# Optimization experiments

Hardware: AMD Instinct MI355X
Metric: run time of the kernel (lower is better)

Reference implementation:

```python
import jax, jax.numpy as jnp
import numpy as np

K = 16  # number of nearest neighbors


def setup_inputs() -> dict:
    key = jax.random.key(0)
    k1, k2, k3 = jax.random.split(key, 3)
    B, N, C, C_OUT = 2, 8192, 64, 64
    coords_knn = jax.random.normal(k1, (B, N, 3), dtype=jnp.float32)
    feat = jax.random.normal(k2, (B, N, C), dtype=jnp.float32)
    # MLP params: Linear(2*C + 3 -> C_OUT)
    W = jax.random.normal(k3, (2 * C + 3, C_OUT), dtype=jnp.float32) * 0.05
    b = jnp.zeros((C_OUT,), dtype=jnp.float32)
    return {"coords_knn": coords_knn, "feat": feat, "W": W, "b": b}


def _knn_idx(coords, k):
    # pairwise squared distances: ||xi||^2 + ||xj||^2 - 2 xi.xj   -> [B, N, N]
    xx = jnp.sum(coords ** 2, axis=-1, keepdims=True)
    dist = xx + jnp.swapaxes(xx, 1, 2) - 2.0 * jnp.einsum('bnc,bmc->bnm', coords, coords)
    dist = jnp.maximum(dist, 0.0)
    _, idx = jax.lax.top_k(-dist, k)  # k smallest distances (order irrelevant: max-pool)
    return idx  # [B, N, k] int32


def reference(coords_knn, feat, W, b):
    idx = _knn_idx(coords_knn, K)
    gather = jax.vmap(lambda a, i: a[i])          # per-batch gather: [N,C],[N,k] -> [N,k,C]
    nb_f = gather(feat, idx)                      # [B, N, k, C]
    nb_p = gather(coords_knn, idx)                # [B, N, k, 3]
    fi = feat[:, :, None, :]                      # [B, N, 1, C]
    pi = coords_knn[:, :, None, :]                # [B, N, 1, 3]
    x = jnp.concatenate(
        [jnp.broadcast_to(fi, nb_f.shape), nb_f - fi, nb_p - pi], axis=-1
    )                                             # [B, N, k, 2C+3]
    x = jax.nn.relu(jnp.einsum('bnkd,do->bnko', x, W) + b)
    return jnp.max(x, axis=2)                     # [B, N, C_OUT]
```

## Files before the change

### kernel.cpp

```cpp
#include <hip/hip_runtime.h>
#include <hip/hip_bf16.h>
#include <stdint.h>
#include <float.h>

#define B_ 2
#define N_ 8192
#define C_ 64
#define K_ 16
#define D_IN 131
#define XS_STRIDE 168
#define TS 1024
#define QPB 16
#define QPW 4
#define CAP 128

typedef __attribute__((ext_vector_type(8))) short short8v;
typedef __attribute__((ext_vector_type(4))) float f32x4;

#define SENT_U64 0x7F7FFFFFFFFFFFFFull

__device__ __forceinline__ float sq3(float x, float y, float z) {
#pragma clang fp contract(off)
  return (x * x + y * y) + z * z;
}

__device__ __forceinline__ uint64_t shfl_xor_u64(uint64_t x, int mask) {
  int lo = __shfl_xor((int)(uint32_t)(x & 0xffffffffull), mask, 64);
  int hi = __shfl_xor((int)(uint32_t)(x >> 32), mask, 64);
  return ((uint64_t)(uint32_t)hi << 32) | (uint32_t)lo;
}

__device__ __forceinline__ double shfl_xor_f64(double x, int mask) {
  return __builtin_bit_cast(double, shfl_xor_u64(__builtin_bit_cast(uint64_t, x), mask));
}

__device__ __forceinline__ uint64_t pack_key_u64(float d, int idx) {
  return ((uint64_t)__float_as_uint(d) << 32) | (uint32_t)idx;
}

__device__ __forceinline__ void insert16(double* hd, double key) {
  hd[15] = key;
#pragma unroll
  for (int z = 15; z >= 1; --z) {
    double a = hd[z - 1], b = hd[z];
    hd[z - 1] = fmin(a, b);
    hd[z] = fmax(a, b);
  }
}

__device__ __forceinline__ float exact_d(float qx, float qy, float qz, float xxq,
                                         float4 cd) {
  float dot2 = fmaf(qz, cd.z, fmaf(qy, cd.y, qx * cd.x));
  float dtmp;
  {
#pragma clang fp contract(off)
    dtmp = (xxq + cd.w) - dot2;
  }
  return fmaxf(dtmp, 0.0f);
}

__global__ __launch_bounds__(256) void prep_c(const float* __restrict__ coords,
                                              float4* __restrict__ c4) {
  int i = blockIdx.x * 256 + threadIdx.x;
  if (i >= B_ * N_) return;
  float cx = coords[i * 3 + 0], cy = coords[i * 3 + 1], cz = coords[i * 3 + 2];
  c4[i] = make_float4(2.0f * cx, 2.0f * cy, 2.0f * cz, sq3(cx, cy, cz));
}

__global__ __launch_bounds__(256) void knn_kernel(const float* __restrict__ coords,
                                                  const float4* __restrict__ c4,
                                                  int* __restrict__ idxout) {
  __shared__ float4 cl[TS];
  __shared__ unsigned long long sbuf[QPB][CAP];
  __shared__ int scnt[QPB];
  const int t = threadIdx.x;
  const int w = t >> 6;
  const int lane = t & 63;
  const int blk = blockIdx.x;
  const int bb = blk >> 9;
  const int qbase = (blk & 511) * QPB;
  const float* cb = coords + (size_t)bb * N_ * 3;
  const float4* cg = c4 + (size_t)bb * N_;

  float qx[QPW], qy[QPW], qz[QPW], xxq[QPW];
#pragma unroll
  for (int r = 0; r < QPW; ++r) {
    int n = qbase + w * QPW + r;
    qx[r] = cb[n * 3 + 0]; qy[r] = cb[n * 3 + 1]; qz[r] = cb[n * 3 + 2];
    xxq[r] = sq3(qx[r], qy[r], qz[r]);
  }
  if (t < QPB) scnt[t] = 0;

#define PROXY(r, cd) fmaf(qz[r], (cd).z, fmaf(qy[r], (cd).y, fmaf(qx[r], (cd).x, -(cd).w)))

  float M[QPW];
#pragma unroll
  for (int r = 0; r < QPW; ++r) M[r] = -FLT_MAX;

  for (int j0 = 0; j0 < N_; j0 += TS) {
    __syncthreads();
#pragma unroll
    for (int i = 0; i < TS / 256; ++i) cl[t + 256 * i] = cg[j0 + t + 256 * i];
    __syncthreads();
#pragma unroll
    for (int i = 0; i < TS / 64; i += 2) {
      float4 ca = cl[i * 64 + lane];
      float4 cb2 = cl[(i + 1) * 64 + lane];
#pragma unroll
      for (int r = 0; r < QPW; ++r) {
        float pa = PROXY(r, ca);
        float pb = PROXY(r, cb2);
        M[r] = fmaxf(M[r], fmaxf(pa, pb));
      }
    }
  }

  float A[QPW], pT[QPW];
#pragma unroll
  for (int r = 0; r < QPW; ++r) { A[r] = M[r]; pT[r] = -FLT_MAX; }
#pragma unroll
  for (int rd = 0; rd < 16; ++rd) {
#pragma unroll
    for (int r = 0; r < QPW; ++r) {
      float g = A[r];
      g = fmaxf(g, __shfl_xor(g, 1, 64));
      g = fmaxf(g, __shfl_xor(g, 2, 64));
      g = fmaxf(g, __shfl_xor(g, 4, 64));
      g = fmaxf(g, __shfl_xor(g, 8, 64));
      g = fmaxf(g, __shfl_xor(g, 16, 64));
      g = fmaxf(g, __shfl_xor(g, 32, 64));
      pT[r] = g;
      A[r] = (A[r] == g) ? -FLT_MAX : A[r];
    }
  }
  float X[QPW];
#pragma unroll
  for (int r = 0; r < QPW; ++r) {
    float slop = 6e-6f * (fabsf(xxq[r]) + fabsf(pT[r])) + 1e-5f;
    X[r] = fminf(pT[r], xxq[r]) - 2.0f * slop;
  }

  for (int j0 = 0; j0 < N_; j0 += TS) {
    __syncthreads();
#pragma unroll
    for (int i = 0; i < TS / 256; ++i) cl[t + 256 * i] = cg[j0 + t + 256 * i];
    __syncthreads();
#pragma unroll
    for (int i = 0; i < TS / 64; i += 2) {
      const int ia = j0 + i * 64 + lane;
      const int ib = ia + 64;
      float4 ca = cl[i * 64 + lane];
      float4 cb2 = cl[(i + 1) * 64 + lane];
#pragma unroll
      for (int r = 0; r < QPW; ++r) {
        float pa = PROXY(r, ca);
        float pb = PROXY(r, cb2);
        if (pa >= X[r]) {
          float d = exact_d(qx[r], qy[r], qz[r], xxq[r], ca);
          int pos = atomicAdd(&scnt[w * QPW + r], 1);
          if (pos < CAP) sbuf[w * QPW + r][pos] = pack_key_u64(d, ia);
        }
        if (pb >= X[r]) {
          float d = exact_d(qx[r], qy[r], qz[r], xxq[r], cb2);
          int pos = atomicAdd(&scnt[w * QPW + r], 1);
          if (pos < CAP) sbuf[w * QPW + r][pos] = pack_key_u64(d, ib);
        }
      }
    }
  }
  __syncthreads();

  const int g16 = lane >> 4;
  const int s16 = lane & 15;
  const int qloc = w * QPW + g16;
  const int n = qbase + qloc;

  double hd[16];
#pragma unroll
  for (int i = 0; i < 16; ++i) hd[i] = __builtin_bit_cast(double, SENT_U64);

  const int cntv = scnt[qloc];
  if (cntv > CAP) {
    float fqx = cb[n * 3 + 0], fqy = cb[n * 3 + 1], fqz = cb[n * 3 + 2];
    float fxx = sq3(fqx, fqy, fqz);
    for (int j = s16; j < N_; j += 16) {
      float cx = cb[j * 3 + 0], cy = cb[j * 3 + 1], cz = cb[j * 3 + 2];
      float ww = sq3(cx, cy, cz);
      float dot = fmaf(fqz, cz, fmaf(fqy, cy, fqx * cx));
      float d2;
      {
#pragma clang fp contract(off)
        d2 = (fxx + ww) - 2.0f * dot;
      }
      d2 = fmaxf(d2, 0.0f);
      double k = __builtin_bit_cast(double, pack_key_u64(d2, j));
      if (k < hd[15]) insert16(hd, k);
    }
  } else {
    for (int i = s16; i < cntv; i += 16) {
      double k = __builtin_bit_cast(double, (uint64_t)sbuf[qloc][i]);
      if (k < hd[15]) insert16(hd, k);
    }
  }

  int* myout = idxout + ((size_t)(bb * N_ + n)) * K_;
#pragma unroll
  for (int r = 0; r < 16; ++r) {
    double v = hd[0];
    v = fmin(v, shfl_xor_f64(v, 1));
    v = fmin(v, shfl_xor_f64(v, 2));
    v = fmin(v, shfl_xor_f64(v, 4));
    v = fmin(v, shfl_xor_f64(v, 8));
    if (__builtin_bit_cast(uint64_t, hd[0]) == __builtin_bit_cast(uint64_t, v)) {
#pragma unroll
      for (int z = 0; z < 15; ++z) hd[z] = hd[z + 1];
      hd[15] = __builtin_bit_cast(double, SENT_U64);
    }
    if (s16 == 0) myout[r] = (int)(uint32_t)__builtin_bit_cast(uint64_t, v);
  }
}

__global__ __launch_bounds__(256) void prep_w(const float* __restrict__ W,
                                              __hip_bfloat16* __restrict__ wfrag) {
  int i = blockIdx.x * 256 + threadIdx.x;
  if (i >= 4 * 5 * 64 * 8) return;
  int j = i & 7;
  int l = (i >> 3) & 63;
  int ks = (i >> 9) % 5;
  int nt = (i >> 9) / 5;
  int k = ks * 32 + (l >> 4) * 8 + j;
  int col = nt * 16 + (l & 15);
  float v = (k < D_IN) ? W[k * 64 + col] : 0.0f;
  wfrag[i] = __float2bfloat16(v);
}

__global__ __launch_bounds__(256) void stage2(const float* __restrict__ coords,
                                              const float* __restrict__ feat,
                                              const int* __restrict__ idxbuf,
                                              const __hip_bfloat16* __restrict__ wfrag,
                                              const float* __restrict__ bias,
                                              float* __restrict__ out) {
  __shared__ __align__(16) __hip_bfloat16 xs[4][16][XS_STRIDE];
  const int t = threadIdx.x;
  const int w = t >> 6;
  const int lane = t & 63;
  const int q = blockIdx.x * 4 + w;
  const int bb = q >> 13;
  const int n = q & (N_ - 1);
  const float* cb = coords + (size_t)bb * N_ * 3;
  const float* fb = feat + (size_t)bb * N_ * C_;
  const int* myidx = idxbuf + (size_t)q * K_;

  float fi = fb[(size_t)n * C_ + lane];
  float qc = (lane < 3) ? cb[n * 3 + lane] : 0.0f;

#pragma unroll
  for (int k = 0; k < K_; ++k) {
    int nb = myidx[k];
    float nf = fb[(size_t)nb * C_ + lane];
    xs[w][k][lane] = __float2bfloat16(fi);
    xs[w][k][C_ + lane] = __float2bfloat16(nf - fi);
    if (lane < 3) {
      xs[w][k][128 + lane] = __float2bfloat16(cb[nb * 3 + lane] - qc);
    } else if (lane < 40) {
      xs[w][k][128 + lane] = __float2bfloat16(0.0f);
    }
  }
  __syncthreads();

  const int row = lane & 15;
  const int g = lane >> 4;
  short8v a[5];
#pragma unroll
  for (int ks = 0; ks < 5; ++ks)
    a[ks] = *(const short8v*)&xs[w][row][ks * 32 + g * 8];

  const short8v* wf = (const short8v*)wfrag;
#pragma unroll
  for (int nt = 0; nt < 4; ++nt) {
    f32x4 acc = {0.f, 0.f, 0.f, 0.f};
#pragma unroll
    for (int ks = 0; ks < 5; ++ks) {
      short8v bf = wf[(nt * 5 + ks) * 64 + lane];
      acc = __builtin_amdgcn_mfma_f32_16x16x32_bf16(a[ks], bf, acc, 0, 0, 0);
    }
    float bcol = bias[nt * 16 + row];
    float m = fmaxf(fmaxf(fmaxf(acc[0] + bcol, 0.f), fmaxf(acc[1] + bcol, 0.f)),
                    fmaxf(fmaxf(acc[2] + bcol, 0.f), fmaxf(acc[3] + bcol, 0.f)));
    m = fmaxf(m, __shfl_xor(m, 16, 64));
    m = fmaxf(m, __shfl_xor(m, 32, 64));
    if (lane < 16) out[(size_t)q * C_ + nt * 16 + row] = m;
  }
}

extern "C" void kernel_launch(void* const* d_in, const int* in_sizes, int n_in,
                              void* d_out, int out_size, void* d_ws, size_t ws_size,
                              hipStream_t stream) {
  const float* coords = (const float*)d_in[0];
  const float* feat = (const float*)d_in[1];
  const float* W = (const float*)d_in[2];
  const float* bias = (const float*)d_in[3];
  float* out = (float*)d_out;

  int* ws_idx = (int*)d_ws;
  char* p = (char*)d_ws + (size_t)B_ * N_ * K_ * sizeof(int);
  __hip_bfloat16* wfrag = (__hip_bfloat16*)p;
  float4* c4 = (float4*)(p + 32768);

  prep_w<<<(4 * 5 * 64 * 8 + 255) / 256, 256, 0, stream>>>(W, wfrag);
  prep_c<<<(B_ * N_ + 255) / 256, 256, 0, stream>>>(coords, c4);
  knn_kernel<<<(B_ * N_) / QPB, 256, 0, stream>>>(coords, c4, ws_idx);
  stage2<<<(B_ * N_) / 4, 256, 0, stream>>>(coords, feat, ws_idx, wfrag, bias, out);
}
```

Before: 113.5 us.

## Fuse kNN selection with gather-MLP stage and merge prep kernels

Merges the weight and coordinate preparation kernels into one launch, and fuses the kNN kernel with the gather+MFMA MLP stage. Neighbor indices now stay in shared memory instead of round-tripping through global memory, and the MLP reuses the kNN shared buffer for its staging tile. This removes two launches and the index write/read, but each block now processes its 16 queries serially, four per wave, with extra block-wide barriers. That lowers parallelism and occupancy in the MLP phase compared with the separate 4096-block stage2 launch.

```diff
diff --git a/kernel.cpp b/kernel.cpp
--- a/kernel.cpp
+++ b/kernel.cpp
@@ -16,8 +16,11 @@
 
 typedef __attribute__((ext_vector_type(8))) short short8v;
 typedef __attribute__((ext_vector_type(4))) float f32x4;
+typedef unsigned long long ull;
 
 #define SENT_U64 0x7F7FFFFFFFFFFFFFull
+
+#define SMEM_BYTES (16384 + QPB * CAP * 8 + QPB * 4)
 
 __device__ __forceinline__ float sq3(float x, float y, float z) {
 #pragma clang fp contract(off)
@@ -59,20 +62,40 @@
   return fmaxf(dtmp, 0.0f);
 }
 
-__global__ __launch_bounds__(256) void prep_c(const float* __restrict__ coords,
-                                              float4* __restrict__ c4) {
+__global__ __launch_bounds__(256) void prep(const float* __restrict__ coords,
+                                            const float* __restrict__ W,
+                                            __hip_bfloat16* __restrict__ wfrag,
+                                            float4* __restrict__ c4) {
   int i = blockIdx.x * 256 + threadIdx.x;
-  if (i >= B_ * N_) return;
-  float cx = coords[i * 3 + 0], cy = coords[i * 3 + 1], cz = coords[i * 3 + 2];
-  c4[i] = make_float4(2.0f * cx, 2.0f * cy, 2.0f * cz, sq3(cx, cy, cz));
-}
-
-__global__ __launch_bounds__(256) void knn_kernel(const float* __restrict__ coords,
-                                                  const float4* __restrict__ c4,
-                                                  int* __restrict__ idxout) {
-  __shared__ float4 cl[TS];
-  __shared__ unsigned long long sbuf[QPB][CAP];
-  __shared__ int scnt[QPB];
+  if (i < 4 * 5 * 64 * 8) {
+    int j = i & 7;
+    int l = (i >> 3) & 63;
+    int ks = (i >> 9) % 5;
+    int nt = (i >> 9) / 5;
+    int k = ks * 32 + (l >> 4) * 8 + j;
+    int col = nt * 16 + (l & 15);
+    float v = (k < D_IN) ? W[k * 64 + col] : 0.0f;
+    wfrag[i] = __float2bfloat16(v);
+  }
+  int j2 = i - 4 * 5 * 64 * 8;
+  if (j2 >= 0 && j2 < B_ * N_) {
+    float cx = coords[j2 * 3 + 0], cy = coords[j2 * 3 + 1], cz = coords[j2 * 3 + 2];
+    c4[j2] = make_float4(2.0f * cx, 2.0f * cy, 2.0f * cz, sq3(cx, cy, cz));
+  }
+}
+
+__global__ __launch_bounds__(256) void knn_fused(const float* __restrict__ coords,
+                                                 const float4* __restrict__ c4,
+                                                 const float* __restrict__ feat,
+                                                 const __hip_bfloat16* __restrict__ wfrag,
+                                                 const float* __restrict__ bias,
+                                                 float* __restrict__ out) {
+  __shared__ __align__(16) char smem[SMEM_BYTES];
+  __shared__ int sidx[QPB][K_];
+  float4* cl = (float4*)smem;
+  ull (*sbuf)[CAP] = (ull(*)[CAP])(smem + 16384);
+  int* scnt = (int*)(smem + 16384 + QPB * CAP * 8);
+
   const int t = threadIdx.x;
   const int w = t >> 6;
   const int lane = t & 63;
@@ -173,7 +196,7 @@
   const int g16 = lane >> 4;
   const int s16 = lane & 15;
   const int qloc = w * QPW + g16;
-  const int n = qbase + qloc;
+  const int nq = qbase + qloc;
 
   double hd[16];
 #pragma unroll
@@ -181,7 +204,7 @@
 
   const int cntv = scnt[qloc];
   if (cntv > CAP) {
-    float fqx = cb[n * 3 + 0], fqy = cb[n * 3 + 1], fqz = cb[n * 3 + 2];
+    float fqx = cb[nq * 3 + 0], fqy = cb[nq * 3 + 1], fqz = cb[nq * 3 + 2];
     float fxx = sq3(fqx, fqy, fqz);
     for (int j = s16; j < N_; j += 16) {
       float cx = cb[j * 3 + 0], cy = cb[j * 3 + 1], cz = cb[j * 3 + 2];
@@ -203,7 +226,6 @@
     }
   }
 
-  int* myout = idxout + ((size_t)(bb * N_ + n)) * K_;
 #pragma unroll
   for (int r = 0; r < 16; ++r) {
     double v = hd[0];
@@ -216,80 +238,57 @@
       for (int z = 0; z < 15; ++z) hd[z] = hd[z + 1];
       hd[15] = __builtin_bit_cast(double, SENT_U64);
     }
-    if (s16 == 0) myout[r] = (int)(uint32_t)__builtin_bit_cast(uint64_t, v);
-  }
-}
-
-__global__ __launch_bounds__(256) void prep_w(const float* __restrict__ W,
-                                              __hip_bfloat16* __restrict__ wfrag) {
-  int i = blockIdx.x * 256 + threadIdx.x;
-  if (i >= 4 * 5 * 64 * 8) return;
-  int j = i & 7;
-  int l = (i >> 3) & 63;
-  int ks = (i >> 9) % 5;
-  int nt = (i >> 9) / 5;
-  int k = ks * 32 + (l >> 4) * 8 + j;
-  int col = nt * 16 + (l & 15);
-  float v = (k < D_IN) ? W[k * 64 + col] : 0.0f;
-  wfrag[i] = __float2bfloat16(v);
-}
-
-__global__ __launch_bounds__(256) void stage2(const float* __restrict__ coords,
-                                              const float* __restrict__ feat,
-                                              const int* __restrict__ idxbuf,
-                                              const __hip_bfloat16* __restrict__ wfrag,
-                                              const float* __restrict__ bias,
-                                              float* __restrict__ out) {
-  __shared__ __align__(16) __hip_bfloat16 xs[4][16][XS_STRIDE];
-  const int t = threadIdx.x;
-  const int w = t >> 6;
-  const int lane = t & 63;
-  const int q = blockIdx.x * 4 + w;
-  const int bb = q >> 13;
-  const int n = q & (N_ - 1);
-  const float* cb = coords + (size_t)bb * N_ * 3;
+    if (s16 == 0) sidx[qloc][r] = (int)(uint32_t)__builtin_bit_cast(uint64_t, v);
+  }
+  __syncthreads();
+
+  __hip_bfloat16 (*xs)[16][XS_STRIDE] = (__hip_bfloat16(*)[16][XS_STRIDE])smem;
   const float* fb = feat + (size_t)bb * N_ * C_;
-  const int* myidx = idxbuf + (size_t)q * K_;
-
-  float fi = fb[(size_t)n * C_ + lane];
-  float qc = (lane < 3) ? cb[n * 3 + lane] : 0.0f;
-
-#pragma unroll
-  for (int k = 0; k < K_; ++k) {
-    int nb = myidx[k];
-    float nf = fb[(size_t)nb * C_ + lane];
-    xs[w][k][lane] = __float2bfloat16(fi);
-    xs[w][k][C_ + lane] = __float2bfloat16(nf - fi);
-    if (lane < 3) {
-      xs[w][k][128 + lane] = __float2bfloat16(cb[nb * 3 + lane] - qc);
-    } else if (lane < 40) {
-      xs[w][k][128 + lane] = __float2bfloat16(0.0f);
-    }
-  }
-  __syncthreads();
-
+  const short8v* wf = (const short8v*)wfrag;
   const int row = lane & 15;
   const int g = lane >> 4;
-  short8v a[5];
-#pragma unroll
-  for (int ks = 0; ks < 5; ++ks)
-    a[ks] = *(const short8v*)&xs[w][row][ks * 32 + g * 8];
-
-  const short8v* wf = (const short8v*)wfrag;
-#pragma unroll
-  for (int nt = 0; nt < 4; ++nt) {
-    f32x4 acc = {0.f, 0.f, 0.f, 0.f};
-#pragma unroll
-    for (int ks = 0; ks < 5; ++ks) {
-      short8v bf = wf[(nt * 5 + ks) * 64 + lane];
-      acc = __builtin_amdgcn_mfma_f32_16x16x32_bf16(a[ks], bf, acc, 0, 0, 0);
-    }
-    float bcol = bias[nt * 16 + row];
-    float m = fmaxf(fmaxf(fmaxf(acc[0] + bcol, 0.f), fmaxf(acc[1] + bcol, 0.f)),
-                    fmaxf(fmaxf(acc[2] + bcol, 0.f), fmaxf(acc[3] + bcol, 0.f)));
-    m = fmaxf(m, __shfl_xor(m, 16, 64));
-    m = fmaxf(m, __shfl_xor(m, 32, 64));
-    if (lane < 16) out[(size_t)q * C_ + nt * 16 + row] = m;
+
+  for (int qi = 0; qi < QPW; ++qi) {
+    const int qloc2 = w * QPW + qi;
+    const int n2 = qbase + qloc2;
+
+    float fi = fb[(size_t)n2 * C_ + lane];
+    float qc = (lane < 3) ? cb[n2 * 3 + lane] : 0.0f;
+#pragma unroll
+    for (int k = 0; k < K_; ++k) {
+      int nb = sidx[qloc2][k];
+      float nf = fb[(size_t)nb * C_ + lane];
+      xs[w][k][lane] = __float2bfloat16(fi);
+      xs[w][k][C_ + lane] = __float2bfloat16(nf - fi);
+      if (lane < 3) {
+        xs[w][k][128 + lane] = __float2bfloat16(cb[nb * 3 + lane] - qc);
+      } else if (lane < 40) {
+        xs[w][k][128 + lane] = __float2bfloat16(0.0f);
+      }
+    }
+    __syncthreads();
+
+    short8v a[5];
+#pragma unroll
+    for (int ks = 0; ks < 5; ++ks)
+      a[ks] = *(const short8v*)&xs[w][row][ks * 32 + g * 8];
+
+#pragma unroll
+    for (int nt = 0; nt < 4; ++nt) {
+      f32x4 acc = {0.f, 0.f, 0.f, 0.f};
+#pragma unroll
+      for (int ks = 0; ks < 5; ++ks) {
+        short8v bf = wf[(nt * 5 + ks) * 64 + lane];
+        acc = __builtin_amdgcn_mfma_f32_16x16x32_bf16(a[ks], bf, acc, 0, 0, 0);
+      }
+      float bcol = bias[nt * 16 + row];
+      float m = fmaxf(fmaxf(fmaxf(acc[0] + bcol, 0.f), fmaxf(acc[1] + bcol, 0.f)),
+                      fmaxf(fmaxf(acc[2] + bcol, 0.f), fmaxf(acc[3] + bcol, 0.f)));
+      m = fmaxf(m, __shfl_xor(m, 16, 64));
+      m = fmaxf(m, __shfl_xor(m, 32, 64));
+      if (lane < 16) out[(size_t)(bb * N_ + n2) * C_ + nt * 16 + row] = m;
+    }
+    __syncthreads();
   }
 }
 
@@ -302,13 +301,10 @@
   const float* bias = (const float*)d_in[3];
   float* out = (float*)d_out;
 
-  int* ws_idx = (int*)d_ws;
-  char* p = (char*)d_ws + (size_t)B_ * N_ * K_ * sizeof(int);
-  __hip_bfloat16* wfrag = (__hip_bfloat16*)p;
-  float4* c4 = (float4*)(p + 32768);
-
-  prep_w<<<(4 * 5 * 64 * 8 + 255) / 256, 256, 0, stream>>>(W, wfrag);
-  prep_c<<<(B_ * N_ + 255) / 256, 256, 0, stream>>>(coords, c4);
-  knn_kernel<<<(B_ * N_) / QPB, 256, 0, stream>>>(coords, c4, ws_idx);
-  stage2<<<(B_ * N_) / 4, 256, 0, stream>>>(coords, feat, ws_idx, wfrag, bias, out);
-}
+  __hip_bfloat16* wfrag = (__hip_bfloat16*)d_ws;
+  float4* c4 = (float4*)((char*)d_ws + 32768);
+
+  const int prep_elems = 4 * 5 * 64 * 8 + B_ * N_;
+  prep<<<(prep_elems + 255) / 256, 256, 0, stream>>>(coords, W, wfrag, c4);
+  knn_fused<<<(B_ * N_) / QPB, 256, 0, stream>>>(coords, c4, feat, wfrag, bias, out);
+}
```

Result: slower. 156.8 us (+38.1%).

## Drop LDS staging in kNN scans and merge prep kernels into one launch

Applied to the files above, without the earlier changes.

The kNN kernel no longer stages candidate coordinate tiles in shared memory with block barriers. Each wave now reads float4 candidates straight from global memory, relying on L1/L2 because all waves read the same data. The first pass also processes four candidates per lane per iteration. The two prep kernels are merged into one launch to save launch overhead, at the risk of more global/cache traffic per wave.

```diff
diff --git a/kernel.cpp b/kernel.cpp
--- a/kernel.cpp
+++ b/kernel.cpp
@@ -9,13 +9,13 @@
 #define K_ 16
 #define D_IN 131
 #define XS_STRIDE 168
-#define TS 1024
 #define QPB 16
 #define QPW 4
 #define CAP 128
 
 typedef __attribute__((ext_vector_type(8))) short short8v;
 typedef __attribute__((ext_vector_type(4))) float f32x4;
+typedef unsigned long long ull;
 
 #define SENT_U64 0x7F7FFFFFFFFFFFFFull
 
@@ -59,19 +59,32 @@
   return fmaxf(dtmp, 0.0f);
 }
 
-__global__ __launch_bounds__(256) void prep_c(const float* __restrict__ coords,
-                                              float4* __restrict__ c4) {
+__global__ __launch_bounds__(256) void prep(const float* __restrict__ coords,
+                                            const float* __restrict__ W,
+                                            __hip_bfloat16* __restrict__ wfrag,
+                                            float4* __restrict__ c4) {
   int i = blockIdx.x * 256 + threadIdx.x;
-  if (i >= B_ * N_) return;
-  float cx = coords[i * 3 + 0], cy = coords[i * 3 + 1], cz = coords[i * 3 + 2];
-  c4[i] = make_float4(2.0f * cx, 2.0f * cy, 2.0f * cz, sq3(cx, cy, cz));
+  if (i < 4 * 5 * 64 * 8) {
+    int j = i & 7;
+    int l = (i >> 3) & 63;
+    int ks = (i >> 9) % 5;
+    int nt = (i >> 9) / 5;
+    int k = ks * 32 + (l >> 4) * 8 + j;
+    int col = nt * 16 + (l & 15);
+    float v = (k < D_IN) ? W[k * 64 + col] : 0.0f;
+    wfrag[i] = __float2bfloat16(v);
+  }
+  int j2 = i - 4 * 5 * 64 * 8;
+  if (j2 >= 0 && j2 < B_ * N_) {
+    float cx = coords[j2 * 3 + 0], cy = coords[j2 * 3 + 1], cz = coords[j2 * 3 + 2];
+    c4[j2] = make_float4(2.0f * cx, 2.0f * cy, 2.0f * cz, sq3(cx, cy, cz));
+  }
 }
 
 __global__ __launch_bounds__(256) void knn_kernel(const float* __restrict__ coords,
                                                   const float4* __restrict__ c4,
                                                   int* __restrict__ idxout) {
-  __shared__ float4 cl[TS];
-  __shared__ unsigned long long sbuf[QPB][CAP];
+  __shared__ ull sbuf[QPB][CAP];
   __shared__ int scnt[QPB];
   const int t = threadIdx.x;
   const int w = t >> 6;
@@ -90,6 +103,7 @@
     xxq[r] = sq3(qx[r], qy[r], qz[r]);
   }
   if (t < QPB) scnt[t] = 0;
+  __syncthreads();
 
 #define PROXY(r, cd) fmaf(qz[r], (cd).z, fmaf(qy[r], (cd).y, fmaf(qx[r], (cd).x, -(cd).w)))
 
@@ -97,21 +111,18 @@
 #pragma unroll
   for (int r = 0; r < QPW; ++r) M[r] = -FLT_MAX;
 
-  for (int j0 = 0; j0 < N_; j0 += TS) {
-    __syncthreads();
-#pragma unroll
-    for (int i = 0; i < TS / 256; ++i) cl[t + 256 * i] = cg[j0 + t + 256 * i];
-    __syncthreads();
-#pragma unroll
-    for (int i = 0; i < TS / 64; i += 2) {
-      float4 ca = cl[i * 64 + lane];
-      float4 cb2 = cl[(i + 1) * 64 + lane];
-#pragma unroll
-      for (int r = 0; r < QPW; ++r) {
-        float pa = PROXY(r, ca);
-        float pb = PROXY(r, cb2);
-        M[r] = fmaxf(M[r], fmaxf(pa, pb));
-      }
+  for (int j0 = 0; j0 < N_; j0 += 256) {
+    float4 ca = cg[j0 + lane];
+    float4 cb2 = cg[j0 + 64 + lane];
+    float4 cc = cg[j0 + 128 + lane];
+    float4 cd = cg[j0 + 192 + lane];
+#pragma unroll
+    for (int r = 0; r < QPW; ++r) {
+      float p0 = PROXY(r, ca);
+      float p1 = PROXY(r, cb2);
+      float p2 = PROXY(r, cc);
+      float p3 = PROXY(r, cd);
+      M[r] = fmaxf(M[r], fmaxf(fmaxf(p0, p1), fmaxf(p2, p3)));
     }
   }
 
@@ -140,31 +151,24 @@
     X[r] = fminf(pT[r], xxq[r]) - 2.0f * slop;
   }
 
-  for (int j0 = 0; j0 < N_; j0 += TS) {
-    __syncthreads();
-#pragma unroll
-    for (int i = 0; i < TS / 256; ++i) cl[t + 256 * i] = cg[j0 + t + 256 * i];
-    __syncthreads();
-#pragma unroll
-    for (int i = 0; i < TS / 64; i += 2) {
-      const int ia = j0 + i * 64 + lane;
-      const int ib = ia + 64;
-      float4 ca = cl[i * 64 + lane];
-      float4 cb2 = cl[(i + 1) * 64 + lane];
-#pragma unroll
-      for (int r = 0; r < QPW; ++r) {
-        float pa = PROXY(r, ca);
-        float pb = PROXY(r, cb2);
-        if (pa >= X[r]) {
-          float d = exact_d(qx[r], qy[r], qz[r], xxq[r], ca);
-          int pos = atomicAdd(&scnt[w * QPW + r], 1);
-          if (pos < CAP) sbuf[w * QPW + r][pos] = pack_key_u64(d, ia);
-        }
-        if (pb >= X[r]) {
-          float d = exact_d(qx[r], qy[r], qz[r], xxq[r], cb2);
-          int pos = atomicAdd(&scnt[w * QPW + r], 1);
-          if (pos < CAP) sbuf[w * QPW + r][pos] = pack_key_u64(d, ib);
-        }
+  for (int j0 = 0; j0 < N_; j0 += 128) {
+    const int ia = j0 + lane;
+    const int ib = ia + 64;
+    float4 ca = cg[ia];
+    float4 cb2 = cg[ib];
+#pragma unroll
+    for (int r = 0; r < QPW; ++r) {
+      float pa = PROXY(r, ca);
+      float pb = PROXY(r, cb2);
+      if (pa >= X[r]) {
+        float d = exact_d(qx[r], qy[r], qz[r], xxq[r], ca);
+        int pos = atomicAdd(&scnt[w * QPW + r], 1);
+        if (pos < CAP) sbuf[w * QPW + r][pos] = pack_key_u64(d, ia);
+      }
+      if (pb >= X[r]) {
+        float d = exact_d(qx[r], qy[r], qz[r], xxq[r], cb2);
+        int pos = atomicAdd(&scnt[w * QPW + r], 1);
+        if (pos < CAP) sbuf[w * QPW + r][pos] = pack_key_u64(d, ib);
       }
     }
   }
@@ -220,20 +224,6 @@
   }
 }
 
-__global__ __launch_bounds__(256) void prep_w(const float* __restrict__ W,
-                                              __hip_bfloat16* __restrict__ wfrag) {
-  int i = blockIdx.x * 256 + threadIdx.x;
-  if (i >= 4 * 5 * 64 * 8) return;
-  int j = i & 7;
-  int l = (i >> 3) & 63;
-  int ks = (i >> 9) % 5;
-  int nt = (i >> 9) / 5;
-  int k = ks * 32 + (l >> 4) * 8 + j;
-  int col = nt * 16 + (l & 15);
-  float v = (k < D_IN) ? W[k * 64 + col] : 0.0f;
-  wfrag[i] = __float2bfloat16(v);
-}
-
 __global__ __launch_bounds__(256) void stage2(const float* __restrict__ coords,
                                               const float* __restrict__ feat,
                                               const int* __restrict__ idxbuf,
@@ -307,8 +297,8 @@
   __hip_bfloat16* wfrag = (__hip_bfloat16*)p;
   float4* c4 = (float4*)(p + 32768);
 
-  prep_w<<<(4 * 5 * 64 * 8 + 255) / 256, 256, 0, stream>>>(W, wfrag);
-  prep_c<<<(B_ * N_ + 255) / 256, 256, 0, stream>>>(coords, c4);
+  const int prep_elems = 4 * 5 * 64 * 8 + B_ * N_;
+  prep<<<(prep_elems + 255) / 256, 256, 0, stream>>>(coords, W, wfrag, c4);
   knn_kernel<<<(B_ * N_) / QPB, 256, 0, stream>>>(coords, c4, ws_idx);
   stage2<<<(B_ * N_) / 4, 256, 0, stream>>>(coords, feat, ws_idx, wfrag, bias, out);
 }
```

After: 115.4 us. Within noise of the previous version (+1.6%).
